# Performance work log

Hardware: AMD Instinct MI355X
Metric: run time of the kernel (lower is better)

## Reference

```python
import jax, jax.numpy as jnp
import numpy as np

NUM_FIELDS = 40
EMBED_DIM = 128
BATCH = 1024
NUM_IX = NUM_FIELDS * (NUM_FIELDS - 1) // 2  # 780


def _pair_indices(num_fields):
    row, col = [], []
    for i in range(num_fields - 1):
        for j in range(i + 1, num_fields):
            row.append(i)
            col.append(j)
    return np.asarray(row, dtype=np.int32), np.asarray(col, dtype=np.int32)


def setup_inputs() -> dict:
    key = jax.random.key(0)
    k1, k2 = jax.random.split(key)
    x = jax.random.normal(k1, (BATCH, NUM_FIELDS, EMBED_DIM), dtype=jnp.float32)
    # 'mat' kernel: (embed_dim, num_ix, embed_dim), random_normal init
    kernel = jax.random.normal(k2, (EMBED_DIM, NUM_IX, EMBED_DIM), dtype=jnp.float32) * 0.05
    return {"x": x, "kernel": kernel}


def reference(x, kernel) -> jnp.ndarray:
    # x: (B, F, D); kernel: (D, num_ix, D)
    row, col = _pair_indices(x.shape[1])
    p = x[:, row, :]  # (B, num_ix, D)
    q = x[:, col, :]  # (B, num_ix, D)
    # Original: tmp[b,e,n] = sum_d p[b,n,d]*kernel[e,n,d]; kp[b,n] = sum_e tmp[b,e,n]*q[b,n,e]
    # Fused contraction, never materializing the (B, D, num_ix, D) tensor:
    kp = jnp.einsum('bnd,end,bne->bn', p, kernel, q)
    return kp  # (B, num_ix)
```

## Files before the change

kernel.cpp:

```cpp
#include <hip/hip_runtime.h>

#define NF 40
#define ED 128
#define NB 1024
#define NIX 780
#define XROW (NF * ED)
#define KROW (NIX * ED)
#define XB_BYTES (NB * NF * ED * 2)
#define KB_BYTES (NIX * ED * ED * 2)
#define WS_NEED (XB_BYTES + KB_BYTES)

typedef __attribute__((ext_vector_type(8))) short bf16x8;
typedef __attribute__((ext_vector_type(4))) float f32x4;
typedef __attribute__((ext_vector_type(4))) unsigned short ushx4;
typedef __attribute__((ext_vector_type(8))) unsigned short ushx8;

__device__ __forceinline__ unsigned short f2bf(float x) {
  unsigned int u = __float_as_uint(x);
  u = (u + 0x7FFFu + ((u >> 16) & 1u)) >> 16;
  return (unsigned short)u;
}
__device__ __forceinline__ float bf2f(unsigned short h) {
  return __uint_as_float(((unsigned int)h) << 16);
}

#define GLOAD16(gsrc, ldst)                                                    \
  __builtin_amdgcn_global_load_lds(                                            \
      (const __attribute__((address_space(1))) void*)(gsrc),                   \
      (__attribute__((address_space(3))) void*)(ldst), 16, 0, 0)

__global__ void cvt_fused(const float* __restrict__ x, const float* __restrict__ kr,
                          unsigned short* __restrict__ xb, unsigned short* __restrict__ kb) {
  const int blk = blockIdx.x;
  if (blk < 2560) {
    const size_t g = ((size_t)blk * 256 + threadIdx.x) * 8;
    float4 a = *reinterpret_cast<const float4*>(x + g);
    float4 b = *reinterpret_cast<const float4*>(x + g + 4);
    ushx8 h;
    h[0] = f2bf(a.x); h[1] = f2bf(a.y); h[2] = f2bf(a.z); h[3] = f2bf(a.w);
    h[4] = f2bf(b.x); h[5] = f2bf(b.y); h[6] = f2bf(b.z); h[7] = f2bf(b.w);
    *reinterpret_cast<ushx8*>(xb + g) = h;
  } else {
    const size_t g = ((size_t)(blk - 2560) * 256 + threadIdx.x) * 4;
    const int d = (int)(g & 127);
    const size_t t = g >> 7;
    const int e = (int)(t & 127);
    const int n = (int)(t >> 7);
    float4 v = *reinterpret_cast<const float4*>(kr + ((size_t)e * NIX + n) * ED + d);
    ushx4 h;
    h[0] = f2bf(v.x); h[1] = f2bf(v.y); h[2] = f2bf(v.z); h[3] = f2bf(v.w);
    *reinterpret_cast<ushx4*>(kb + g) = h;
  }
}

__launch_bounds__(256, 4)
__global__ void opn_ws(const unsigned short* __restrict__ xb,
                       const unsigned short* __restrict__ kb,
                       float* __restrict__ out) {
  __shared__ unsigned short S[16384];
  __shared__ float scratch[4][32];

  const int n = blockIdx.x;
  const int tid = threadIdx.x;
  const int lane = tid & 63;
  const int w = tid >> 6;
  const int lm = lane & 15;
  const int lq = lane >> 4;
  const int col8 = lm * 8;

  int fi = 0, base = 0;
  while (base + (NF - 1 - fi) <= n) { base += NF - 1 - fi; ++fi; }
  const int fj = fi + 1 + (n - base);

  {
    const unsigned short* ks = kb + (size_t)n * (ED * ED);
    #pragma unroll
    for (int j = 0; j < 8; ++j) {
      const int chunk = j * 4 + w;
      const int r = chunk * 4 + lq;
      const int c = col8 ^ ((r & 7) << 3);
      GLOAD16(ks + r * ED + c, S + chunk * 512);
    }
  }
  __syncthreads();

  bf16x8 afr[4][2];
  #pragma unroll
  for (int kk = 0; kk < 4; ++kk)
    #pragma unroll
    for (int f = 0; f < 2; ++f) {
      const int r = w * 32 + f * 16 + lm;
      afr[kk][f] = *reinterpret_cast<const bf16x8*>(
          &S[r * ED + ((kk * 32 + lq * 8) ^ ((r & 7) << 3))]);
    }
  #pragma unroll
  for (int kk = 0; kk < 4; ++kk)
    #pragma unroll
    for (int f = 0; f < 2; ++f)
      asm volatile("" : "+v"(afr[kk][f]));
  __syncthreads();

  unsigned short* Plds = S;
  unsigned short* Qlds = S + 4096;

  const int b0base = blockIdx.y * 256;

  #pragma unroll 1
  for (int t = 0; t < 8; ++t) {
    const int b0 = b0base + t * 32;

    #pragma unroll
    for (int j = 0; j < 2; ++j) {
      const int chunk = j * 4 + w;
      const int r = chunk * 4 + lq;
      const int c = col8 ^ ((r & 7) << 3);
      const size_t xoff = (size_t)(b0 + r) * XROW + c;
      GLOAD16(xb + xoff + (size_t)fi * ED, Plds + chunk * 512);
      GLOAD16(xb + xoff + (size_t)fj * ED, Qlds + chunk * 512);
    }
    __syncthreads();

    f32x4 acc[2][2];
    #pragma unroll
    for (int f = 0; f < 2; ++f)
      #pragma unroll
      for (int nt = 0; nt < 2; ++nt)
        acc[f][nt] = (f32x4){0.f, 0.f, 0.f, 0.f};

    __builtin_amdgcn_s_setprio(1);
    #pragma unroll
    for (int kk = 0; kk < 4; ++kk) {
      #pragma unroll
      for (int nt = 0; nt < 2; ++nt) {
        const int pb = nt * 16 + lm;
        bf16x8 pfr = *reinterpret_cast<const bf16x8*>(
            &Plds[pb * ED + ((kk * 32 + lq * 8) ^ ((pb & 7) << 3))]);
        #pragma unroll
        for (int f = 0; f < 2; ++f)
          acc[f][nt] = __builtin_amdgcn_mfma_f32_16x16x32_bf16(afr[kk][f], pfr, acc[f][nt], 0, 0, 0);
      }
    }
    __builtin_amdgcn_s_setprio(0);

    float s[2];
    #pragma unroll
    for (int nt = 0; nt < 2; ++nt) {
      const int qrow = nt * 16 + lm;
      float t0 = 0.f, t1 = 0.f, t2 = 0.f, t3 = 0.f;
      #pragma unroll
      for (int f = 0; f < 2; ++f) {
        const int c = (w * 32 + f * 16 + lq * 4) ^ ((qrow & 7) << 3);
        ushx4 q4 = *reinterpret_cast<const ushx4*>(&Qlds[qrow * ED + c]);
        t0 = fmaf(acc[f][nt][0], bf2f(q4[0]), t0);
        t1 = fmaf(acc[f][nt][1], bf2f(q4[1]), t1);
        t2 = fmaf(acc[f][nt][2], bf2f(q4[2]), t2);
        t3 = fmaf(acc[f][nt][3], bf2f(q4[3]), t3);
      }
      float sv = (t0 + t1) + (t2 + t3);
      sv += __shfl_xor(sv, 16);
      sv += __shfl_xor(sv, 32);
      s[nt] = sv;
    }
    if (lq == 0) {
      scratch[w][lm] = s[0];
      scratch[w][16 + lm] = s[1];
    }
    __syncthreads();

    if (tid < 32) {
      const int b = tid;
      float r = (scratch[0][b] + scratch[1][b]) + (scratch[2][b] + scratch[3][b]);
      out[(size_t)(b0 + b) * NIX + n] = r;
    }
  }
}

__device__ __forceinline__ int swz_fb(int row, int col) {
  return row * 128 + (col ^ ((row & 7) << 3));
}

__launch_bounds__(256, 2)
__global__ void opn_fb(const float* __restrict__ x,
                       const float* __restrict__ kern,
                       float* __restrict__ out) {
  __shared__ unsigned short Klds[128 * 128];
  __shared__ unsigned short Plds[64 * 128];
  __shared__ unsigned short Qlds[64 * 132];

  const int n = blockIdx.x;
  const int tid = threadIdx.x;
  const int lane = tid & 63;
  const int w = tid >> 6;
  const int lm = lane & 15;
  const int lq = lane >> 4;

  int fi = 0, base = 0;
  while (base + (NF - 1 - fi) <= n) { base += NF - 1 - fi; ++fi; }
  const int fj = fi + 1 + (n - base);

  {
    const int r8 = tid >> 5;
    const int d0 = (tid & 31) * 4;
    const float* kbp = kern + (size_t)n * ED + d0;
    #pragma unroll
    for (int p = 0; p < 16; ++p) {
      int e = p * 8 + r8;
      float4 v = *reinterpret_cast<const float4*>(kbp + (size_t)e * KROW);
      ushx4 h;
      h[0] = f2bf(v.x); h[1] = f2bf(v.y); h[2] = f2bf(v.z); h[3] = f2bf(v.w);
      *reinterpret_cast<ushx4*>(&Klds[swz_fb(e, d0)]) = h;
    }
  }
  __syncthreads();

  bf16x8 bfr[4][8];
  #pragma unroll
  for (int kk = 0; kk < 4; ++kk)
    #pragma unroll
    for (int f = 0; f < 8; ++f)
      bfr[kk][f] = *reinterpret_cast<const bf16x8*>(
          &Klds[swz_fb(f * 16 + lm, kk * 32 + lq * 8)]);

  const int r8 = tid >> 5;
  const int c4 = (tid & 31) * 4;

  for (int t = 0; t < 8; ++t) {
    const int b0 = blockIdx.y * 512 + t * 64;
    __syncthreads();
    #pragma unroll
    for (int p = 0; p < 8; ++p) {
      int r = p * 8 + r8;
      const float* xbp = x + (size_t)(b0 + r) * XROW + c4;
      float4 vp = *reinterpret_cast<const float4*>(xbp + fi * ED);
      ushx4 hp;
      hp[0] = f2bf(vp.x); hp[1] = f2bf(vp.y); hp[2] = f2bf(vp.z); hp[3] = f2bf(vp.w);
      *reinterpret_cast<ushx4*>(&Plds[swz_fb(r, c4)]) = hp;
      float4 vq = *reinterpret_cast<const float4*>(xbp + fj * ED);
      ushx4 hq;
      hq[0] = f2bf(vq.x); hq[1] = f2bf(vq.y); hq[2] = f2bf(vq.z); hq[3] = f2bf(vq.w);
      *reinterpret_cast<ushx4*>(&Qlds[r * 132 + c4]) = hq;
    }
    __syncthreads();

    f32x4 acc[8];
    #pragma unroll
    for (int f = 0; f < 8; ++f) acc[f] = (f32x4){0.f, 0.f, 0.f, 0.f};
    #pragma unroll
    for (int kk = 0; kk < 4; ++kk) {
      bf16x8 a = *reinterpret_cast<const bf16x8*>(
          &Plds[swz_fb(w * 16 + lm, kk * 32 + lq * 8)]);
      #pragma unroll
      for (int f = 0; f < 8; ++f)
        acc[f] = __builtin_amdgcn_mfma_f32_16x16x32_bf16(a, bfr[kk][f], acc[f], 0, 0, 0);
    }

    #pragma unroll
    for (int r = 0; r < 4; ++r) {
      const int bl = w * 16 + lq * 4 + r;
      float s = 0.f;
      #pragma unroll
      for (int f = 0; f < 8; ++f)
        s = fmaf(acc[f][r], bf2f(Qlds[bl * 132 + f * 16 + lm]), s);
      s += __shfl_xor(s, 1);
      s += __shfl_xor(s, 2);
      s += __shfl_xor(s, 4);
      s += __shfl_xor(s, 8);
      if (lm == 0) out[(size_t)(b0 + bl) * NIX + n] = s;
    }
  }
}

extern "C" void kernel_launch(void* const* d_in, const int* in_sizes, int n_in,
                              void* d_out, int out_size, void* d_ws, size_t ws_size,
                              hipStream_t stream) {
  const float* x = (const float*)d_in[0];
  const float* kern = (const float*)d_in[1];
  float* out = (float*)d_out;
  (void)in_sizes; (void)n_in; (void)out_size;

  if (ws_size >= (size_t)WS_NEED) {
    unsigned short* xb = (unsigned short*)d_ws;
    unsigned short* kbuf = (unsigned short*)((char*)d_ws + XB_BYTES);
    cvt_fused<<<15040, 256, 0, stream>>>(x, kern, xb, kbuf);
    dim3 grid(NIX, 4, 1);
    opn_ws<<<grid, 256, 0, stream>>>(xb, kbuf, out);
  } else {
    dim3 grid(NIX, 2, 1);
    opn_fb<<<grid, 256, 0, stream>>>(x, kern, out);
  }
}
```

Baseline: 74.50 us.

## Process 2x2 field-pair tiles per block to reuse P/Q loads

```diff
diff --git a/kernel.cpp b/kernel.cpp
--- a/kernel.cpp
+++ b/kernel.cpp
@@ -4,6 +4,8 @@
 #define ED 128
 #define NB 1024
 #define NIX 780
+#define NC 20
+#define CROSS 190
 #define XROW (NF * ED)
 #define KROW (NIX * ED)
 #define XB_BYTES (NB * NF * ED * 2)
@@ -53,14 +55,17 @@
   }
 }
 
-__launch_bounds__(256, 4)
+__device__ __forceinline__ int nix_of(int i, int j) {
+  return i * (2 * NF - i - 1) / 2 + (j - i - 1);
+}
+
+__launch_bounds__(256, 2)
 __global__ void opn_ws(const unsigned short* __restrict__ xb,
                        const unsigned short* __restrict__ kb,
                        float* __restrict__ out) {
-  __shared__ unsigned short S[16384];
-  __shared__ float scratch[4][32];
-
-  const int n = blockIdx.x;
+  __shared__ unsigned short S[32768];
+  __shared__ float scratch[4][4][32];
+
   const int tid = threadIdx.x;
   const int lane = tid & 63;
   const int w = tid >> 6;
@@ -68,81 +73,112 @@
   const int lq = lane >> 4;
   const int col8 = lm * 8;
 
-  int fi = 0, base = 0;
-  while (base + (NF - 1 - fi) <= n) { base += NF - 1 - fi; ++fi; }
-  const int fj = fi + 1 + (n - base);
+  const int bid = blockIdx.x;
+  int fP0, fP1, fQ0, fQ1, np, nq;
+  if (bid < CROSS) {
+    int ca = 0, base = 0;
+    while (base + (NC - 1 - ca) <= bid) { base += NC - 1 - ca; ++ca; }
+    const int cb = ca + 1 + (bid - base);
+    fP0 = 2 * ca; fP1 = fP0 + 1; fQ0 = 2 * cb; fQ1 = fQ0 + 1;
+    np = 2; nq = 2;
+  } else {
+    const int c = bid - CROSS;
+    fP0 = 2 * c; fP1 = fP0; fQ0 = fP0 + 1; fQ1 = fQ0;
+    np = 1; nq = 1;
+  }
+  const int n00 = nix_of(fP0, fQ0);
+  const int n01 = (nq == 2) ? n00 + 1 : n00;
+  const int n10 = (np == 2) ? nix_of(fP1, fQ0) : n00;
 
   {
-    const unsigned short* ks = kb + (size_t)n * (ED * ED);
+    const unsigned short* kA = kb + (size_t)n00 * (ED * ED);
+    const unsigned short* kBp = kb + (size_t)n01 * (ED * ED);
     #pragma unroll
     for (int j = 0; j < 8; ++j) {
       const int chunk = j * 4 + w;
       const int r = chunk * 4 + lq;
       const int c = col8 ^ ((r & 7) << 3);
-      GLOAD16(ks + r * ED + c, S + chunk * 512);
-    }
-  }
-  __syncthreads();
-
-  bf16x8 afr[4][2];
+      GLOAD16(kA + r * ED + c, S + chunk * 512);
+      GLOAD16(kBp + r * ED + c, S + 16384 + chunk * 512);
+    }
+  }
+  __syncthreads();
+
+  bf16x8 kfr00[4][2], kfr01[4][2], kfr10[4][2], kfr11[4][2];
   #pragma unroll
   for (int kk = 0; kk < 4; ++kk)
     #pragma unroll
     for (int f = 0; f < 2; ++f) {
       const int r = w * 32 + f * 16 + lm;
-      afr[kk][f] = *reinterpret_cast<const bf16x8*>(
-          &S[r * ED + ((kk * 32 + lq * 8) ^ ((r & 7) << 3))]);
-    }
-  #pragma unroll
-  for (int kk = 0; kk < 4; ++kk)
-    #pragma unroll
-    for (int f = 0; f < 2; ++f)
-      asm volatile("" : "+v"(afr[kk][f]));
-  __syncthreads();
-
-  unsigned short* Plds = S;
-  unsigned short* Qlds = S + 4096;
-
-  const int b0base = blockIdx.y * 256;
-
-  #pragma unroll 1
-  for (int t = 0; t < 8; ++t) {
-    const int b0 = b0base + t * 32;
-
-    #pragma unroll
-    for (int j = 0; j < 2; ++j) {
+      const int off = r * ED + ((kk * 32 + lq * 8) ^ ((r & 7) << 3));
+      kfr00[kk][f] = *reinterpret_cast<const bf16x8*>(&S[off]);
+      kfr01[kk][f] = *reinterpret_cast<const bf16x8*>(&S[16384 + off]);
+    }
+  #pragma unroll
+  for (int kk = 0; kk < 4; ++kk)
+    #pragma unroll
+    for (int f = 0; f < 2; ++f) {
+      asm volatile("" : "+v"(kfr00[kk][f]));
+      asm volatile("" : "+v"(kfr01[kk][f]));
+    }
+  __syncthreads();
+
+  {
+    const unsigned short* kA = kb + (size_t)n10 * (ED * ED);
+    const unsigned short* kBp = kb + (size_t)(n10 + (nq == 2 ? 1 : 0)) * (ED * ED);
+    #pragma unroll
+    for (int j = 0; j < 8; ++j) {
       const int chunk = j * 4 + w;
       const int r = chunk * 4 + lq;
       const int c = col8 ^ ((r & 7) << 3);
-      const size_t xoff = (size_t)(b0 + r) * XROW + c;
-      GLOAD16(xb + xoff + (size_t)fi * ED, Plds + chunk * 512);
-      GLOAD16(xb + xoff + (size_t)fj * ED, Qlds + chunk * 512);
-    }
-    __syncthreads();
-
+      GLOAD16(kA + r * ED + c, S + chunk * 512);
+      GLOAD16(kBp + r * ED + c, S + 16384 + chunk * 512);
+    }
+  }
+  __syncthreads();
+  #pragma unroll
+  for (int kk = 0; kk < 4; ++kk)
+    #pragma unroll
+    for (int f = 0; f < 2; ++f) {
+      const int r = w * 32 + f * 16 + lm;
+      const int off = r * ED + ((kk * 32 + lq * 8) ^ ((r & 7) << 3));
+      kfr10[kk][f] = *reinterpret_cast<const bf16x8*>(&S[off]);
+      kfr11[kk][f] = *reinterpret_cast<const bf16x8*>(&S[16384 + off]);
+    }
+  #pragma unroll
+  for (int kk = 0; kk < 4; ++kk)
+    #pragma unroll
+    for (int f = 0; f < 2; ++f) {
+      asm volatile("" : "+v"(kfr10[kk][f]));
+      asm volatile("" : "+v"(kfr11[kk][f]));
+    }
+  __syncthreads();
+
+  unsigned short* PlP0 = S;
+  unsigned short* PlP1 = S + 4096;
+  unsigned short* PlQ0 = S + 8192;
+  unsigned short* PlQ1 = S + 12288;
+
+  const int b0base = blockIdx.y * 256;
+
+  auto pair_compute = [&](const bf16x8 (&kf)[4][2], const bf16x8 (&pf)[2][4],
+                          const unsigned short* Qp, int pidx) {
     f32x4 acc[2][2];
     #pragma unroll
     for (int f = 0; f < 2; ++f)
       #pragma unroll
       for (int nt = 0; nt < 2; ++nt)
         acc[f][nt] = (f32x4){0.f, 0.f, 0.f, 0.f};
-
     __builtin_amdgcn_s_setprio(1);
     #pragma unroll
-    for (int kk = 0; kk < 4; ++kk) {
-      #pragma unroll
-      for (int nt = 0; nt < 2; ++nt) {
-        const int pb = nt * 16 + lm;
-        bf16x8 pfr = *reinterpret_cast<const bf16x8*>(
-            &Plds[pb * ED + ((kk * 32 + lq * 8) ^ ((pb & 7) << 3))]);
+    for (int kk = 0; kk < 4; ++kk)
+      #pragma unroll
+      for (int nt = 0; nt < 2; ++nt)
         #pragma unroll
         for (int f = 0; f < 2; ++f)
-          acc[f][nt] = __builtin_amdgcn_mfma_f32_16x16x32_bf16(afr[kk][f], pfr, acc[f][nt], 0, 0, 0);
-      }
-    }
+          acc[f][nt] = __builtin_amdgcn_mfma_f32_16x16x32_bf16(
+              kf[kk][f], pf[nt][kk], acc[f][nt], 0, 0, 0);
     __builtin_amdgcn_s_setprio(0);
-
-    float s[2];
     #pragma unroll
     for (int nt = 0; nt < 2; ++nt) {
       const int qrow = nt * 16 + lm;
@@ -150,7 +186,7 @@
       #pragma unroll
       for (int f = 0; f < 2; ++f) {
         const int c = (w * 32 + f * 16 + lq * 4) ^ ((qrow & 7) << 3);
-        ushx4 q4 = *reinterpret_cast<const ushx4*>(&Qlds[qrow * ED + c]);
+        ushx4 q4 = *reinterpret_cast<const ushx4*>(&Qp[qrow * ED + c]);
         t0 = fmaf(acc[f][nt][0], bf2f(q4[0]), t0);
         t1 = fmaf(acc[f][nt][1], bf2f(q4[1]), t1);
         t2 = fmaf(acc[f][nt][2], bf2f(q4[2]), t2);
@@ -159,18 +195,72 @@
       float sv = (t0 + t1) + (t2 + t3);
       sv += __shfl_xor(sv, 16);
       sv += __shfl_xor(sv, 32);
-      s[nt] = sv;
-    }
-    if (lq == 0) {
-      scratch[w][lm] = s[0];
-      scratch[w][16 + lm] = s[1];
+      if (lq == 0) scratch[w][pidx][nt * 16 + lm] = sv;
+    }
+  };
+
+  #pragma unroll 1
+  for (int t = 0; t < 8; ++t) {
+    const int b0 = b0base + t * 32;
+
+    #pragma unroll
+    for (int pl = 0; pl < 4; ++pl) {
+      const int fld = (pl == 0) ? fP0 : (pl == 1) ? fP1 : (pl == 2) ? fQ0 : fQ1;
+      #pragma unroll
+      for (int j = 0; j < 2; ++j) {
+        const int chunk = j * 4 + w;
+        const int r = chunk * 4 + lq;
+        const int c = col8 ^ ((r & 7) << 3);
+        GLOAD16(xb + (size_t)(b0 + r) * XROW + (size_t)fld * ED + c,
+                S + pl * 4096 + chunk * 512);
+      }
     }
     __syncthreads();
 
-    if (tid < 32) {
-      const int b = tid;
-      float r = (scratch[0][b] + scratch[1][b]) + (scratch[2][b] + scratch[3][b]);
-      out[(size_t)(b0 + b) * NIX + n] = r;
+    {
+      bf16x8 pf0[2][4];
+      #pragma unroll
+      for (int nt = 0; nt < 2; ++nt)
+        #pragma unroll
+        for (int kk = 0; kk < 4; ++kk) {
+          const int pb = nt * 16 + lm;
+          pf0[nt][kk] = *reinterpret_cast<const bf16x8*>(
+              &PlP0[pb * ED + ((kk * 32 + lq * 8) ^ ((pb & 7) << 3))]);
+        }
+      pair_compute(kfr00, pf0, PlQ0, 0);
+      if (nq == 2) pair_compute(kfr01, pf0, PlQ1, 1);
+    }
+    if (np == 2) {
+      bf16x8 pf1[2][4];
+      #pragma unroll
+      for (int nt = 0; nt < 2; ++nt)
+        #pragma unroll
+        for (int kk = 0; kk < 4; ++kk) {
+          const int pb = nt * 16 + lm;
+          pf1[nt][kk] = *reinterpret_cast<const bf16x8*>(
+              &PlP1[pb * ED + ((kk * 32 + lq * 8) ^ ((pb & 7) << 3))]);
+        }
+      pair_compute(kfr10, pf1, PlQ0, 2);
+      pair_compute(kfr11, pf1, PlQ1, 3);
+    }
+    __syncthreads();
+
+    if (bid < CROSS) {
+      if (tid < 128) {
+        const int pair = tid >> 5;
+        const int b = tid & 31;
+        const float v = (scratch[0][pair][b] + scratch[1][pair][b]) +
+                        (scratch[2][pair][b] + scratch[3][pair][b]);
+        const int nsel = ((pair & 2) ? n10 : n00) + (pair & 1);
+        out[(size_t)(b0 + b) * NIX + nsel] = v;
+      }
+    } else {
+      if (tid < 32) {
+        const int b = tid;
+        const float v = (scratch[0][0][b] + scratch[1][0][b]) +
+                        (scratch[2][0][b] + scratch[3][0][b]);
+        out[(size_t)(b0 + b) * NIX + n00] = v;
+      }
     }
   }
 }
@@ -282,7 +372,7 @@
     unsigned short* xb = (unsigned short*)d_ws;
     unsigned short* kbuf = (unsigned short*)((char*)d_ws + XB_BYTES);
     cvt_fused<<<15040, 256, 0, stream>>>(x, kern, xb, kbuf);
-    dim3 grid(NIX, 4, 1);
+    dim3 grid(CROSS + NC, 4, 1);
     opn_ws<<<grid, 256, 0, stream>>>(xb, kbuf, out);
   } else {
     dim3 grid(NIX, 2, 1);
```

Measured after the change: 82.95 us. +11.3%, slower.
